# Performance work log

Measured on AMD Instinct MI355X. Metric: run time of the kernel, lower is better.

The kernel has to match this reference:

```python
import jax, jax.numpy as jnp
import numpy as np

BATCH = 4_194_304
N_LEVELS = 8
LEVEL_PENALTY_SCALE = 1.0


def setup_inputs() -> dict:
    key = jax.random.key(0)
    k1, k2 = jax.random.split(key)
    predictions = jax.random.normal(k1, (BATCH, N_LEVELS), dtype=jnp.float32)
    targets = jax.random.randint(k2, (BATCH,), 0, N_LEVELS, dtype=jnp.int64)
    return {"predictions": predictions, "targets": targets}


def reference(predictions, targets):
    n_levels = predictions.shape[-1]
    # level_distances[i, j] = |i - j|
    lv = jnp.arange(n_levels)
    level_distances = jnp.abs(lv[:, None] - lv[None, :]).astype(predictions.dtype)

    # per-sample cross entropy (reduction='none')
    logp = jax.nn.log_softmax(predictions, axis=-1)
    ce_loss = -jnp.take_along_axis(logp, targets[:, None], axis=-1)[:, 0]

    # hierarchy penalty: fused gather, no python loop / host sync
    pred_levels = jnp.argmax(predictions, axis=-1)
    penalties = level_distances[targets, pred_levels]

    weighted_loss = ce_loss * (1.0 + LEVEL_PENALTY_SCALE * penalties)
    return jnp.mean(weighted_loss)
```

## Files before the change

### kernel.cpp

```cpp
#include <hip/hip_runtime.h>

#define NBLOCKS 2048
#define TPB 256

__device__ __forceinline__ double block_reduce_d(double x) {
    #pragma unroll
    for (int off = 32; off > 0; off >>= 1)
        x += __shfl_down(x, off, 64);
    __shared__ double lds[TPB / 64];
    const int lane = threadIdx.x & 63;
    const int wid  = threadIdx.x >> 6;
    if (lane == 0) lds[wid] = x;
    __syncthreads();
    if (wid == 0) {
        x = (lane < (TPB / 64)) ? lds[lane] : 0.0;
        #pragma unroll
        for (int off = (TPB / 128); off > 0; off >>= 1)
            x += __shfl_down(x, off, 64);
    }
    return x;
}

__global__ __launch_bounds__(TPB) void hrl_partial(
    const float* __restrict__ pred,
    const int*   __restrict__ tgt,
    double*      __restrict__ partial,
    int batch)
{
    const int tid    = blockIdx.x * TPB + threadIdx.x;
    const int stride = gridDim.x * TPB;

    double acc = 0.0;
    for (int i = tid; i < batch; i += stride) {
        const float4* p = reinterpret_cast<const float4*>(pred) + (size_t)i * 2;
        const float4 a = p[0];
        const float4 b = p[1];
        float v[8] = {a.x, a.y, a.z, a.w, b.x, b.y, b.z, b.w};

        float m = v[0];
        int  am = 0;
        #pragma unroll
        for (int j = 1; j < 8; ++j) {
            if (v[j] > m) { m = v[j]; am = j; }
        }

        const int t = tgt[i];
        float s  = 0.f;
        float vt = 0.f;
        #pragma unroll
        for (int j = 0; j < 8; ++j) {
            s += __expf(v[j] - m);
            vt = (j == t) ? v[j] : vt;
        }

        const float ce  = -(vt - m - __logf(s));
        const float pen = (float)abs(t - am);
        acc += (double)(ce * (1.0f + pen));
    }

    const double bsum = block_reduce_d(acc);
    if (threadIdx.x == 0) partial[blockIdx.x] = bsum;
}

__global__ __launch_bounds__(TPB) void hrl_final(
    const double* __restrict__ partial,
    float*        __restrict__ out,
    int nparts, double inv_batch)
{
    double s = 0.0;
    for (int i = threadIdx.x; i < nparts; i += TPB)
        s += partial[i];
    const double tot = block_reduce_d(s);
    if (threadIdx.x == 0) out[0] = (float)(tot * inv_batch);
}

extern "C" void kernel_launch(void* const* d_in, const int* in_sizes, int n_in,
                              void* d_out, int out_size, void* d_ws, size_t ws_size,
                              hipStream_t stream) {
    const float* pred = (const float*)d_in[0];
    const int*   tgt  = (const int*)d_in[1];
    float*  out = (float*)d_out;
    double* ws  = (double*)d_ws;

    const int batch = in_sizes[0] / 8;

    hrl_partial<<<NBLOCKS, TPB, 0, stream>>>(pred, tgt, ws, batch);
    hrl_final<<<1, TPB, 0, stream>>>(ws, out, NBLOCKS, 1.0 / (double)batch);
}
```

Baseline: 33.51 us.

## Split each row across two lanes for fully coalesced float4 loads

Each row of 8 logits is now handled by a pair of lanes, each loading one float4, so a wavefront reads a contiguous 1 KB span per instruction instead of strided 32-byte rows. Max, argmax, exp-sum and the target logit are combined across the pair with xor shuffles, and each lane adds half the per-row loss. This aims to improve load coalescing, at the cost of extra shuffles and with each lane now fetching the target index redundantly.

```diff
diff --git a/kernel.cpp b/kernel.cpp
--- a/kernel.cpp
+++ b/kernel.cpp
@@ -2,6 +2,8 @@
 
 #define NBLOCKS 2048
 #define TPB 256
+
+typedef float f32x4 __attribute__((ext_vector_type(4)));
 
 __device__ __forceinline__ double block_reduce_d(double x) {
     #pragma unroll
@@ -27,35 +29,50 @@
     double*      __restrict__ partial,
     int batch)
 {
-    const int tid    = blockIdx.x * TPB + threadIdx.x;
-    const int stride = gridDim.x * TPB;
+    const int lane = threadIdx.x & 63;
+    const int half = lane & 1;
+    const int pair = lane >> 1;
+    const int gwave  = (blockIdx.x * TPB + threadIdx.x) >> 6;
+    const int nwaves = (NBLOCKS * TPB) >> 6;
 
     double acc = 0.0;
-    for (int i = tid; i < batch; i += stride) {
-        const float4* p = reinterpret_cast<const float4*>(pred) + (size_t)i * 2;
-        const float4 a = p[0];
-        const float4 b = p[1];
-        float v[8] = {a.x, a.y, a.z, a.w, b.x, b.y, b.z, b.w};
+    for (int base = gwave * 32; base < batch; base += nwaves * 32) {
+        const int r = base + pair;
+        if (r < batch) {
+            const f32x4 v = *(reinterpret_cast<const f32x4*>(pred) + (size_t)r * 2 + half);
+            const int   t = tgt[r];
 
-        float m = v[0];
-        int  am = 0;
-        #pragma unroll
-        for (int j = 1; j < 8; ++j) {
-            if (v[j] > m) { m = v[j]; am = j; }
+            float m4 = v.x; int a4 = 0;
+            if (v.y > m4) { m4 = v.y; a4 = 1; }
+            if (v.z > m4) { m4 = v.z; a4 = 2; }
+            if (v.w > m4) { m4 = v.w; a4 = 3; }
+            a4 += half * 4;
+
+            const float om = __shfl_xor(m4, 1, 64);
+            const int   oa = __shfl_xor(a4, 1, 64);
+            const float mlo = half ? om : m4;
+            const float mhi = half ? m4 : om;
+            const int   alo = half ? oa : a4;
+            const int   ahi = half ? a4 : oa;
+            const float m  = fmaxf(mlo, mhi);
+            const int   am = (mhi > mlo) ? ahi : alo;
+
+            float s4 = __expf(v.x - m) + __expf(v.y - m)
+                     + __expf(v.z - m) + __expf(v.w - m);
+            const float s = s4 + __shfl_xor(s4, 1, 64);
+
+            const int tb = t - half * 4;
+            float vt4 = 0.f;
+            vt4 = (tb == 0) ? v.x : vt4;
+            vt4 = (tb == 1) ? v.y : vt4;
+            vt4 = (tb == 2) ? v.z : vt4;
+            vt4 = (tb == 3) ? v.w : vt4;
+            const float vt = vt4 + __shfl_xor(vt4, 1, 64);
+
+            const float ce = -(vt - m - __logf(s));
+            int d = t - am; d = (d < 0) ? -d : d;
+            acc += (double)(ce * (1.0f + (float)d)) * 0.5;
         }
-
-        const int t = tgt[i];
-        float s  = 0.f;
-        float vt = 0.f;
-        #pragma unroll
-        for (int j = 0; j < 8; ++j) {
-            s += __expf(v[j] - m);
-            vt = (j == t) ? v[j] : vt;
-        }
-
-        const float ce  = -(vt - m - __logf(s));
-        const float pen = (float)abs(t - am);
-        acc += (double)(ce * (1.0f + pen));
     }
 
     const double bsum = block_reduce_d(acc);
```

Measured after the change: 31.98 us. 1.05x faster.
